# Kernel optimization log

Hardware: AMD Instinct MI355X
Metric: run time of the kernel (lower is better)

Reference implementation:

```python
import jax, jax.numpy as jnp
import numpy as np

N_NODES = 50000
N_EDGES = 800000  # undirected edge count E0
D_FEAT = 64
K_STEPS = 10
LAMBDA = 3.0


def setup_inputs() -> dict:
    key = jax.random.key(0)
    k1, k2, k3 = jax.random.split(key, 3)
    x = jax.random.normal(k1, (N_NODES, D_FEAT), dtype=jnp.float32)
    edge_src = jax.random.randint(k2, (N_EDGES,), 0, N_NODES)
    edge_dst = jax.random.randint(k3, (N_EDGES,), 0, N_NODES)
    return {"x": x, "edge_src": edge_src, "edge_dst": edge_dst}


def _forward(x, edge_src, edge_dst):
    N, D = x.shape
    # --- symmetric adjacency (directed edge list, both orientations) ---
    row = jnp.concatenate([edge_src, edge_dst])
    col = jnp.concatenate([edge_dst, edge_src])
    # degree with self loops (fill_diag/add_self_loops weight 1), shared by
    # gcn_norm and inc_norm in the original code
    deg = jax.ops.segment_sum(jnp.ones(row.shape[0], x.dtype), row, num_segments=N) + 1.0
    dis = deg ** -0.5  # deg_inv_sqrt, [N]
    # gcn-normalized adjacency weights D^-1/2 (A+I) D^-1/2
    w = dis[row] * dis[col]          # off-diagonal edge weights [2*E0]
    w_self = dis * dis               # self-loop weights [N]

    def adj_mv(v):  # edge_index @ v
        return jax.ops.segment_sum(w[:, None] * v[col], row, num_segments=N) + w_self[:, None] * v

    # --- normalized incidence matrix (one row per undirected edge) ---
    r = jnp.maximum(edge_src, edge_dst)  # row_index after row>=col mask
    c = jnp.minimum(edge_src, edge_dst)
    a = dis[r]  # +1 entry scaled by deg_inv_sqrt of column r
    b = dis[c]  # -1 entry scaled by deg_inv_sqrt of column c

    def inc_mv(v):  # inc_mat @ v -> [E0, D]
        return a[:, None] * v[r] - b[:, None] * v[c]

    def incT_mv(z):  # inc_mat.t() @ z -> [N, D]
        return (jax.ops.segment_sum(a[:, None] * z, r, num_segments=N)
                - jax.ops.segment_sum(b[:, None] * z, c, num_segments=N))

    def l21_projection(z):
        rn = jnp.linalg.norm(z, axis=1)                 # row L2 norms [E0]
        s = jnp.minimum(rn, LAMBDA)
        s = jnp.where(rn > 0, s / jnp.where(rn > 0, rn, 1.0), s)
        return s[:, None] * z

    hh = x
    z0 = jnp.zeros((edge_src.shape[0], D), x.dtype)

    def step(carry, _):
        xk, zk = carry
        y = 0.25 * hh + 0.75 * adj_mv(xk)
        x_bar = y - 0.25 * incT_mv(zk)
        z_bar = zk + 2.0 * inc_mv(x_bar)
        zk = l21_projection(z_bar)
        xk = y - 0.25 * incT_mv(zk)
        return (xk, zk), None

    (xK, _), _ = jax.lax.scan(step, (x, z0), None, length=K_STEPS)
    return xK


def reference(x, edge_src, edge_dst):
    return _forward(x, edge_src, edge_dst)
```

## Files before the change

kernel.cpp:

```cpp
#include <hip/hip_runtime.h>
#include <hip/hip_fp16.h>
#include <math.h>

constexpr int NN = 50000;
constexpr int NE = 800000;
constexpr int KS = 10;
constexpr float LAM = 3.0f;

constexpr int SCAN_NB = (NN + 255) / 256;
constexpr int NODE_NB = NN * 64 / 256;


__global__ __launch_bounds__(256) void countRC_kernel(
    const int* __restrict__ src, const int* __restrict__ dst,
    int* __restrict__ cR, int* __restrict__ cC) {
  int e = blockIdx.x * 256 + threadIdx.x;
  if (e >= NE) return;
  int s = src[e], d = dst[e];
  int r = s > d ? s : d;
  int c = s > d ? d : s;
  atomicAdd(&cR[r], 1);
  atomicAdd(&cC[c], 1);
}

__global__ __launch_bounds__(256) void dis_kernel(
    const int* __restrict__ cR, const int* __restrict__ cC,
    float* __restrict__ dis) {
  int i = blockIdx.x * 256 + threadIdx.x;
  if (i < NN) dis[i] = 1.0f / sqrtf((float)(cR[i] + cC[i] + 1));
}

__global__ __launch_bounds__(256) void half_copy_kernel(
    const float* __restrict__ X, __half* __restrict__ XH) {
  int i = blockIdx.x * 256 + threadIdx.x;
  if (i >= NN * 16) return;
  float4 v = ((const float4*)X)[i];
  __half2 h0 = __floats2half2_rn(v.x, v.y);
  __half2 h1 = __floats2half2_rn(v.z, v.w);
  uint2 o;
  o.x = *(const unsigned*)&h0;
  o.y = *(const unsigned*)&h1;
  ((uint2*)XH)[i] = o;
}


__global__ __launch_bounds__(256) void scanA_kernel(
    const int* __restrict__ cnt, int* __restrict__ bsum) {
  __shared__ int sm[256];
  int t = threadIdx.x;
  int i = blockIdx.x * 256 + t;
  int v = (i < NN) ? cnt[i] : 0;
  sm[t] = v;
  __syncthreads();
  for (int off = 128; off > 0; off >>= 1) {
    if (t < off) sm[t] += sm[t + off];
    __syncthreads();
  }
  if (t == 0) bsum[blockIdx.x] = sm[0];
}

__global__ __launch_bounds__(256) void scanB_kernel(
    int* __restrict__ bsum, int* __restrict__ boff) {
  __shared__ int sm[256];
  int t = threadIdx.x;
  int v = (t < SCAN_NB) ? bsum[t] : 0;
  sm[t] = v;
  __syncthreads();
  for (int off = 1; off < 256; off <<= 1) {
    int a = (t >= off) ? sm[t - off] : 0;
    __syncthreads();
    sm[t] += a;
    __syncthreads();
  }
  if (t < SCAN_NB) boff[t] = sm[t] - v;
}

__global__ __launch_bounds__(256) void scanC_kernel(
    const int* __restrict__ cnt, const int* __restrict__ boff,
    int* __restrict__ ptr, int* __restrict__ cur) {
  __shared__ int sm[256];
  int t = threadIdx.x;
  int i = blockIdx.x * 256 + t;
  int v = (i < NN) ? cnt[i] : 0;
  sm[t] = v;
  __syncthreads();
  for (int off = 1; off < 256; off <<= 1) {
    int a = (t >= off) ? sm[t - off] : 0;
    __syncthreads();
    sm[t] += a;
    __syncthreads();
  }
  if (i < NN) {
    int ex = boff[blockIdx.x] + sm[t] - v;
    ptr[i] = ex;
    cur[i] = ex;
    if (i == NN - 1) ptr[NN] = ex + v;
  }
}

__global__ __launch_bounds__(256) void sortscatter_kernel(
    const int* __restrict__ src, const int* __restrict__ dst,
    const float* __restrict__ dis,
    int* __restrict__ urR, int* __restrict__ uC,
    int2* __restrict__ cb8, int2* __restrict__ cEnt) {
  int e = blockIdx.x * 256 + threadIdx.x;
  if (e >= NE) return;
  int s = src[e], d = dst[e];
  int r = s > d ? s : d;
  int c = s > d ? d : s;
  int p = atomicAdd(&urR[r], 1);
  cb8[p] = make_int2(c, __float_as_int(dis[c]));
  int q = atomicAdd(&uC[c], 1);
  cEnt[q] = make_int2(r, p);
}


template <int FIRST>
__global__ __launch_bounds__(256) void adj_kernel(
    const __half* __restrict__ XH, const float* __restrict__ H,
    const float* __restrict__ U, const float* __restrict__ dis,
    const int* __restrict__ rPtr, const int* __restrict__ cPtr,
    const int2* __restrict__ cEnt, const int2* __restrict__ cb8,
    float* __restrict__ XB, __half* __restrict__ XBh) {
  int w = (int)((blockIdx.x * 256u + threadIdx.x) >> 6);
  if (w >= NN) return;
  int lane = threadIdx.x & 63;
  int g = lane >> 4, l = lane & 15;
  const uint2* XH2 = (const uint2*)XH;
  int rb = rPtr[w], lenR = rPtr[w + 1] - rb;
  int cb = cPtr[w], lenC = cPtr[w + 1] - cb;
  int total = lenR + lenC;
  int lr1 = lenR > 0 ? lenR - 1 : 0;
  int lc1 = lenC > 0 ? lenC - 1 : 0;
  float ax = 0.f, ay = 0.f, az = 0.f, aw = 0.f;

#define ADJ_FETCH(T, NB, WT)                                         \
  {                                                                  \
    int tr = (T) < lr1 ? (T) : lr1;                                  \
    int tc = (T) - lenR; tc = tc > 0 ? tc : 0; tc = tc < lc1 ? tc : lc1; \
    int2 rcv = cb8[rb + tr];                                         \
    int2 ce = cEnt[cb + tc];                                         \
    bool isR = (T) < lenR;                                           \
    NB = isR ? rcv.x : ce.x;                                         \
    WT = isR ? __int_as_float(rcv.y) : dis[ce.x];                    \
  }
#define ADJ_ACC(XV, W)                                               \
  {                                                                  \
    float2 p = __half22float2(*(const __half2*)&XV.x);               \
    float2 q = __half22float2(*(const __half2*)&XV.y);               \
    ax = fmaf(W, p.x, ax); ay = fmaf(W, p.y, ay);                    \
    az = fmaf(W, q.x, az); aw = fmaf(W, q.y, aw);                    \
  }

  int t = g;
  for (; t + 12 < total; t += 16) {
    int n0, n1, n2, n3; float w0, w1, w2, w3;
    ADJ_FETCH(t, n0, w0);
    ADJ_FETCH(t + 4, n1, w1);
    ADJ_FETCH(t + 8, n2, w2);
    ADJ_FETCH(t + 12, n3, w3);
    uint2 x0 = XH2[n0 * 16 + l];
    uint2 x1 = XH2[n1 * 16 + l];
    uint2 x2 = XH2[n2 * 16 + l];
    uint2 x3 = XH2[n3 * 16 + l];
    ADJ_ACC(x0, w0);
    ADJ_ACC(x1, w1);
    ADJ_ACC(x2, w2);
    ADJ_ACC(x3, w3);
  }
  for (; t < total; t += 4) {
    int n0; float w0;
    ADJ_FETCH(t, n0, w0);
    uint2 x0 = XH2[n0 * 16 + l];
    ADJ_ACC(x0, w0);
  }
#undef ADJ_FETCH
#undef ADJ_ACC

  ax += __shfl_xor(ax, 16, 64); ay += __shfl_xor(ay, 16, 64);
  az += __shfl_xor(az, 16, 64); aw += __shfl_xor(aw, 16, 64);
  ax += __shfl_xor(ax, 32, 64); ay += __shfl_xor(ay, 32, 64);
  az += __shfl_xor(az, 32, 64); aw += __shfl_xor(aw, 32, 64);
  if (g == 0) {
    float di = dis[w];
    int idx = w * 16 + l;
    uint2 xsu = XH2[idx];
    float2 xsa = __half22float2(*(const __half2*)&xsu.x);
    float2 xsb = __half22float2(*(const __half2*)&xsu.y);
    float4 h4 = ((const float4*)H)[idx];
    float4 y4;
    y4.x = 0.25f * h4.x + 0.75f * di * fmaf(di, xsa.x, ax);
    y4.y = 0.25f * h4.y + 0.75f * di * fmaf(di, xsa.y, ay);
    y4.z = 0.25f * h4.z + 0.75f * di * fmaf(di, xsb.x, az);
    y4.w = 0.25f * h4.w + 0.75f * di * fmaf(di, xsb.y, aw);
    float4 xb;
    if (FIRST) {
      xb = y4;
    } else {
      float4 u4 = ((const float4*)U)[idx];
      xb.x = y4.x - 0.25f * u4.x;
      xb.y = y4.y - 0.25f * u4.y;
      xb.z = y4.z - 0.25f * u4.z;
      xb.w = y4.w - 0.25f * u4.w;
    }
    ((float4*)XB)[idx] = xb;
    __half2 hb0 = __floats2half2_rn(xb.x, xb.y);
    __half2 hb1 = __floats2half2_rn(xb.z, xb.w);
    uint2 ob;
    ob.x = *(const unsigned*)&hb0;
    ob.y = *(const unsigned*)&hb1;
    ((uint2*)XBh)[idx] = ob;
  }
}

template <int FIRST>
__global__ __launch_bounds__(256) void zupd_kernel(
    __half* __restrict__ Z, const __half* __restrict__ XBh,
    const float* __restrict__ dis,
    const int* __restrict__ rPtr, const int2* __restrict__ cb8,
    float* __restrict__ U1) {
  int i = (int)((blockIdx.x * 256u + threadIdx.x) >> 6);
  if (i >= NN) return;
  int w = (i & 1) ? (NN - 1 - (i >> 1)) : (i >> 1);
  int lane = threadIdx.x & 63;
  int g = lane >> 4, l = lane & 15;
  const uint2* X2 = (const uint2*)XBh;
  uint2* Z2 = (uint2*)Z;
  int rb = rPtr[w], re = rPtr[w + 1];
  float a2 = 2.0f * dis[w];
  uint2 xwu = X2[w * 16 + l];
  float2 xwa = __half22float2(*(const __half2*)&xwu.x);
  float2 xwb = __half22float2(*(const __half2*)&xwu.y);
  float tx = a2 * xwa.x, ty = a2 * xwa.y;
  float tz = a2 * xwb.x, tw = a2 * xwb.y;
  float sx = 0.f, sy = 0.f, sz = 0.f, sw = 0.f;

#define Z_PROC(E, CV, XCU, ZU)                                       \
  {                                                                  \
    float b2 = 2.0f * __int_as_float(CV.y);                          \
    float2 xca = __half22float2(*(const __half2*)&XCU.x);            \
    float2 xcb = __half22float2(*(const __half2*)&XCU.y);            \
    float zx, zy, zz, zw;                                            \
    if (FIRST) {                                                     \
      zx = zy = zz = zw = 0.f;                                       \
    } else {                                                         \
      float2 f0 = __half22float2(*(const __half2*)&ZU.x);            \
      float2 f1 = __half22float2(*(const __half2*)&ZU.y);            \
      zx = f0.x; zy = f0.y; zz = f1.x; zw = f1.y;                    \
    }                                                                \
    zx += tx - b2 * xca.x;                                           \
    zy += ty - b2 * xca.y;                                           \
    zz += tz - b2 * xcb.x;                                           \
    zw += tw - b2 * xcb.y;                                           \
    float ss = zx * zx + zy * zy + zz * zz + zw * zw;                \
    ss += __shfl_xor(ss, 1, 64);                                     \
    ss += __shfl_xor(ss, 2, 64);                                     \
    ss += __shfl_xor(ss, 4, 64);                                     \
    ss += __shfl_xor(ss, 8, 64);                                     \
    float rn = sqrtf(ss);                                            \
    float sc = (rn > LAM) ? (LAM / rn) : 1.0f;                       \
    zx *= sc; zy *= sc; zz *= sc; zw *= sc;                          \
    __half2 o0 = __floats2half2_rn(zx, zy);                          \
    __half2 o1 = __floats2half2_rn(zz, zw);                          \
    uint2 outu;                                                      \
    outu.x = *(const unsigned*)&o0;                                  \
    outu.y = *(const unsigned*)&o1;                                  \
    Z2[(E) * 16 + l] = outu;                                         \
    sx += zx; sy += zy; sz += zz; sw += zw;                          \
  }

  int e = rb + g;
  for (; e + 4 < re; e += 8) {
    int2 cv0 = cb8[e];
    int2 cv1 = cb8[e + 4];
    uint2 xc0 = X2[cv0.x * 16 + l];
    uint2 xc1 = X2[cv1.x * 16 + l];
    uint2 zu0, zu1;
    if (!FIRST) {
      zu0 = Z2[e * 16 + l];
      zu1 = Z2[(e + 4) * 16 + l];
    }
    Z_PROC(e, cv0, xc0, zu0);
    Z_PROC(e + 4, cv1, xc1, zu1);
  }
  if (e < re) {
    int2 cv0 = cb8[e];
    uint2 xc0 = X2[cv0.x * 16 + l];
    uint2 zu0;
    if (!FIRST) zu0 = Z2[e * 16 + l];
    Z_PROC(e, cv0, xc0, zu0);
  }
#undef Z_PROC

  sx += __shfl_xor(sx, 16, 64); sy += __shfl_xor(sy, 16, 64);
  sz += __shfl_xor(sz, 16, 64); sw += __shfl_xor(sw, 16, 64);
  sx += __shfl_xor(sx, 32, 64); sy += __shfl_xor(sy, 32, 64);
  sz += __shfl_xor(sz, 32, 64); sw += __shfl_xor(sw, 32, 64);
  if (g == 0) {
    ((float4*)U1)[w * 16 + l] = make_float4(sx, sy, sz, sw);
  }
}

template <int FIRST, int LAST>
__global__ __launch_bounds__(256) void cside_kernel(
    const __half* __restrict__ Z, const float* __restrict__ XB,
    const float* __restrict__ dis,
    const int* __restrict__ cPtr, const int2* __restrict__ cEnt,
    const float* __restrict__ U1, float* __restrict__ U,
    float* __restrict__ Xout, __half* __restrict__ XH) {
  int i = (int)((blockIdx.x * 256u + threadIdx.x) >> 6);
  if (i >= NN) return;
  int w = (i & 1) ? (NN - 1 - (i >> 1)) : (i >> 1);
  int lane = threadIdx.x & 63;
  int g = lane >> 4, l = lane & 15;
  const uint2* Z2 = (const uint2*)Z;
  int cb = cPtr[w], ce = cPtr[w + 1];
  float sx = 0.f, sy = 0.f, sz = 0.f, sw = 0.f;
  int j = cb + g;
  for (; j + 12 < ce; j += 16) {
    int e0 = cEnt[j].y;
    int e1 = cEnt[j + 4].y;
    int e2 = cEnt[j + 8].y;
    int e3 = cEnt[j + 12].y;
    uint2 zu0 = Z2[e0 * 16 + l];
    uint2 zu1 = Z2[e1 * 16 + l];
    uint2 zu2 = Z2[e2 * 16 + l];
    uint2 zu3 = Z2[e3 * 16 + l];
    float2 a0 = __half22float2(*(const __half2*)&zu0.x);
    float2 b0 = __half22float2(*(const __half2*)&zu0.y);
    float2 a1 = __half22float2(*(const __half2*)&zu1.x);
    float2 b1 = __half22float2(*(const __half2*)&zu1.y);
    float2 a2 = __half22float2(*(const __half2*)&zu2.x);
    float2 b2 = __half22float2(*(const __half2*)&zu2.y);
    float2 a3 = __half22float2(*(const __half2*)&zu3.x);
    float2 b3 = __half22float2(*(const __half2*)&zu3.y);
    sx += a0.x + a1.x + a2.x + a3.x;
    sy += a0.y + a1.y + a2.y + a3.y;
    sz += b0.x + b1.x + b2.x + b3.x;
    sw += b0.y + b1.y + b2.y + b3.y;
  }
  for (; j < ce; j += 4) {
    int e0 = cEnt[j].y;
    uint2 zu0 = Z2[e0 * 16 + l];
    float2 a0 = __half22float2(*(const __half2*)&zu0.x);
    float2 b0 = __half22float2(*(const __half2*)&zu0.y);
    sx += a0.x; sy += a0.y; sz += b0.x; sw += b0.y;
  }
  sx += __shfl_xor(sx, 16, 64); sy += __shfl_xor(sy, 16, 64);
  sz += __shfl_xor(sz, 16, 64); sw += __shfl_xor(sw, 16, 64);
  sx += __shfl_xor(sx, 32, 64); sy += __shfl_xor(sy, 32, 64);
  sz += __shfl_xor(sz, 32, 64); sw += __shfl_xor(sw, 32, 64);
  if (g == 0) {
    float di = dis[w];
    int idx = w * 16 + l;
    float4 u1 = ((const float4*)U1)[idx];
    float4 u;
    u.x = di * (u1.x - sx);
    u.y = di * (u1.y - sy);
    u.z = di * (u1.z - sz);
    u.w = di * (u1.w - sw);
    float4 xb = ((const float4*)XB)[idx];
    float4 y4;
    if (FIRST) {
      y4 = xb;
    } else {
      float4 uo = ((const float4*)U)[idx];
      y4.x = xb.x + 0.25f * uo.x;
      y4.y = xb.y + 0.25f * uo.y;
      y4.z = xb.z + 0.25f * uo.z;
      y4.w = xb.w + 0.25f * uo.w;
    }
    float4 o;
    o.x = y4.x - 0.25f * u.x;
    o.y = y4.y - 0.25f * u.y;
    o.z = y4.z - 0.25f * u.z;
    o.w = y4.w - 0.25f * u.w;
    if (LAST) {
      ((float4*)Xout)[idx] = o;
    } else {
      ((float4*)U)[idx] = u;
      __half2 h0 = __floats2half2_rn(o.x, o.y);
      __half2 h1 = __floats2half2_rn(o.z, o.w);
      uint2 oh;
      oh.x = *(const unsigned*)&h0;
      oh.y = *(const unsigned*)&h1;
      ((uint2*)XH)[idx] = oh;
    }
  }
}


extern "C" void kernel_launch(void* const* d_in, const int* in_sizes, int n_in,
                              void* d_out, int out_size, void* d_ws, size_t ws_size,
                              hipStream_t stream) {
  const float* x  = (const float*)d_in[0];
  const int* esrc = (const int*)d_in[1];
  const int* edst = (const int*)d_in[2];
  float* out = (float*)d_out;

  char* base = (char*)d_ws;
  size_t off = 0;
  auto carve = [&](size_t bytes) -> void* {
    void* p = base + off;
    off += (bytes + 255) & ~(size_t)255;
    return p;
  };
  __half* Z   = (__half*)carve((size_t)NE * 64 * 2);
  float* XB   = (float*)carve((size_t)NN * 64 * 4);
  float* U    = (float*)carve((size_t)NN * 64 * 4);
  float* U1   = (float*)carve((size_t)NN * 64 * 4);
  __half* XH  = (__half*)carve((size_t)NN * 64 * 2);
  __half* XBh = (__half*)carve((size_t)NN * 64 * 2);
  float* dis = (float*)carve((size_t)NN * 4);
  int* cR  = (int*)carve((size_t)NN * 4);
  int* cC  = (int*)carve((size_t)NN * 4);
  int* rPtr = (int*)carve((size_t)(NN + 1) * 4);
  int* cPtr = (int*)carve((size_t)(NN + 1) * 4);
  int* urR = (int*)carve((size_t)NN * 4);
  int* uC  = (int*)carve((size_t)NN * 4);
  int* bsum = (int*)carve((size_t)SCAN_NB * 4);
  int* boff = (int*)carve((size_t)SCAN_NB * 4);
  int2* cb8  = (int2*)carve((size_t)(NE + 4) * 8);
  int2* cEnt = (int2*)carve((size_t)(NE + 4) * 8);
  (void)ws_size; (void)in_sizes; (void)n_in; (void)out_size;

  hipMemsetAsync(cR, 0, NN * 4, stream);
  hipMemsetAsync(cC, 0, NN * 4, stream);

  const int edgeGrid = (NE + 255) / 256;
  countRC_kernel<<<edgeGrid, 256, 0, stream>>>(esrc, edst, cR, cC);
  dis_kernel<<<(NN + 255) / 256, 256, 0, stream>>>(cR, cC, dis);
  half_copy_kernel<<<(NN * 16 + 255) / 256, 256, 0, stream>>>(x, XH);
  scanA_kernel<<<SCAN_NB, 256, 0, stream>>>(cR, bsum);
  scanB_kernel<<<1, 256, 0, stream>>>(bsum, boff);
  scanC_kernel<<<SCAN_NB, 256, 0, stream>>>(cR, boff, rPtr, urR);
  scanA_kernel<<<SCAN_NB, 256, 0, stream>>>(cC, bsum);
  scanB_kernel<<<1, 256, 0, stream>>>(bsum, boff);
  scanC_kernel<<<SCAN_NB, 256, 0, stream>>>(cC, boff, cPtr, uC);
  sortscatter_kernel<<<edgeGrid, 256, 0, stream>>>(esrc, edst, dis, urR, uC,
                                                   cb8, cEnt);

  for (int k = 0; k < KS; ++k) {
    if (k == 0)
      adj_kernel<1><<<NODE_NB, 256, 0, stream>>>(XH, x, U, dis, rPtr, cPtr,
                                                 cEnt, cb8, XB, XBh);
    else
      adj_kernel<0><<<NODE_NB, 256, 0, stream>>>(XH, x, U, dis, rPtr, cPtr,
                                                 cEnt, cb8, XB, XBh);

    if (k == 0)
      zupd_kernel<1><<<NODE_NB, 256, 0, stream>>>(Z, XBh, dis, rPtr, cb8, U1);
    else
      zupd_kernel<0><<<NODE_NB, 256, 0, stream>>>(Z, XBh, dis, rPtr, cb8, U1);

    if (k == 0)
      cside_kernel<1, 0><<<NODE_NB, 256, 0, stream>>>(Z, XB, dis, cPtr, cEnt,
                                                      U1, U, out, XH);
    else if (k == KS - 1)
      cside_kernel<0, 1><<<NODE_NB, 256, 0, stream>>>(Z, XB, dis, cPtr, cEnt,
                                                      U1, U, out, XH);
    else
      cside_kernel<0, 0><<<NODE_NB, 256, 0, stream>>>(Z, XB, dis, cPtr, cEnt,
                                                      U1, U, out, XH);
  }
}
```

Before: 1.360 ms.

## Precompute merged adjacency list with weights and deepen zupd unroll

Result: no change. 1.377 ms (+1.3%).

```diff
diff --git a/kernel.cpp b/kernel.cpp
--- a/kernel.cpp
+++ b/kernel.cpp
@@ -114,36 +114,47 @@
   cEnt[q] = make_int2(r, p);
 }
 
+__global__ __launch_bounds__(256) void adjm_kernel(
+    const int* __restrict__ rPtr, const int* __restrict__ cPtr,
+    const int2* __restrict__ cb8, const int2* __restrict__ cEnt,
+    const float* __restrict__ dis, int2* __restrict__ adjM) {
+  int w = (int)((blockIdx.x * 256u + threadIdx.x) >> 6);
+  if (w >= NN) return;
+  int lane = threadIdx.x & 63;
+  int rb = rPtr[w], lenR = rPtr[w + 1] - rb;
+  int cb = cPtr[w], lenC = cPtr[w + 1] - cb;
+  int total = lenR + lenC;
+  int ab = rb + cb;
+  for (int t = lane; t < total; t += 64) {
+    int2 m;
+    if (t < lenR) {
+      m = cb8[rb + t];
+    } else {
+      int rr = cEnt[cb + t - lenR].x;
+      m = make_int2(rr, __float_as_int(dis[rr]));
+    }
+    adjM[ab + t] = m;
+  }
+}
+
 
 template <int FIRST>
 __global__ __launch_bounds__(256) void adj_kernel(
     const __half* __restrict__ XH, const float* __restrict__ H,
     const float* __restrict__ U, const float* __restrict__ dis,
     const int* __restrict__ rPtr, const int* __restrict__ cPtr,
-    const int2* __restrict__ cEnt, const int2* __restrict__ cb8,
+    const int2* __restrict__ adjM,
     float* __restrict__ XB, __half* __restrict__ XBh) {
   int w = (int)((blockIdx.x * 256u + threadIdx.x) >> 6);
   if (w >= NN) return;
   int lane = threadIdx.x & 63;
   int g = lane >> 4, l = lane & 15;
   const uint2* XH2 = (const uint2*)XH;
-  int rb = rPtr[w], lenR = rPtr[w + 1] - rb;
-  int cb = cPtr[w], lenC = cPtr[w + 1] - cb;
-  int total = lenR + lenC;
-  int lr1 = lenR > 0 ? lenR - 1 : 0;
-  int lc1 = lenC > 0 ? lenC - 1 : 0;
+  int rb = rPtr[w], cb = cPtr[w];
+  int ab = rb + cb;
+  int total = rPtr[w + 1] + cPtr[w + 1] - ab;
   float ax = 0.f, ay = 0.f, az = 0.f, aw = 0.f;
 
-#define ADJ_FETCH(T, NB, WT)                                         \
-  {                                                                  \
-    int tr = (T) < lr1 ? (T) : lr1;                                  \
-    int tc = (T) - lenR; tc = tc > 0 ? tc : 0; tc = tc < lc1 ? tc : lc1; \
-    int2 rcv = cb8[rb + tr];                                         \
-    int2 ce = cEnt[cb + tc];                                         \
-    bool isR = (T) < lenR;                                           \
-    NB = isR ? rcv.x : ce.x;                                         \
-    WT = isR ? __int_as_float(rcv.y) : dis[ce.x];                    \
-  }
 #define ADJ_ACC(XV, W)                                               \
   {                                                                  \
     float2 p = __half22float2(*(const __half2*)&XV.x);               \
@@ -154,27 +165,27 @@
 
   int t = g;
   for (; t + 12 < total; t += 16) {
-    int n0, n1, n2, n3; float w0, w1, w2, w3;
-    ADJ_FETCH(t, n0, w0);
-    ADJ_FETCH(t + 4, n1, w1);
-    ADJ_FETCH(t + 8, n2, w2);
-    ADJ_FETCH(t + 12, n3, w3);
-    uint2 x0 = XH2[n0 * 16 + l];
-    uint2 x1 = XH2[n1 * 16 + l];
-    uint2 x2 = XH2[n2 * 16 + l];
-    uint2 x3 = XH2[n3 * 16 + l];
+    int2 m0 = adjM[ab + t];
+    int2 m1 = adjM[ab + t + 4];
+    int2 m2 = adjM[ab + t + 8];
+    int2 m3 = adjM[ab + t + 12];
+    uint2 x0 = XH2[m0.x * 16 + l];
+    uint2 x1 = XH2[m1.x * 16 + l];
+    uint2 x2 = XH2[m2.x * 16 + l];
+    uint2 x3 = XH2[m3.x * 16 + l];
+    float w0 = __int_as_float(m0.y), w1 = __int_as_float(m1.y);
+    float w2 = __int_as_float(m2.y), w3 = __int_as_float(m3.y);
     ADJ_ACC(x0, w0);
     ADJ_ACC(x1, w1);
     ADJ_ACC(x2, w2);
     ADJ_ACC(x3, w3);
   }
   for (; t < total; t += 4) {
-    int n0; float w0;
-    ADJ_FETCH(t, n0, w0);
-    uint2 x0 = XH2[n0 * 16 + l];
+    int2 m0 = adjM[ab + t];
+    uint2 x0 = XH2[m0.x * 16 + l];
+    float w0 = __int_as_float(m0.y);
     ADJ_ACC(x0, w0);
   }
-#undef ADJ_FETCH
 #undef ADJ_ACC
 
   ax += __shfl_xor(ax, 16, 64); ay += __shfl_xor(ay, 16, 64);
@@ -270,20 +281,28 @@
   }
 
   int e = rb + g;
-  for (; e + 4 < re; e += 8) {
+  for (; e + 12 < re; e += 16) {
     int2 cv0 = cb8[e];
     int2 cv1 = cb8[e + 4];
+    int2 cv2 = cb8[e + 8];
+    int2 cv3 = cb8[e + 12];
     uint2 xc0 = X2[cv0.x * 16 + l];
     uint2 xc1 = X2[cv1.x * 16 + l];
-    uint2 zu0, zu1;
+    uint2 xc2 = X2[cv2.x * 16 + l];
+    uint2 xc3 = X2[cv3.x * 16 + l];
+    uint2 zu0, zu1, zu2, zu3;
     if (!FIRST) {
       zu0 = Z2[e * 16 + l];
       zu1 = Z2[(e + 4) * 16 + l];
+      zu2 = Z2[(e + 8) * 16 + l];
+      zu3 = Z2[(e + 12) * 16 + l];
     }
     Z_PROC(e, cv0, xc0, zu0);
     Z_PROC(e + 4, cv1, xc1, zu1);
-  }
-  if (e < re) {
+    Z_PROC(e + 8, cv2, xc2, zu2);
+    Z_PROC(e + 12, cv3, xc3, zu3);
+  }
+  for (; e < re; e += 4) {
     int2 cv0 = cb8[e];
     uint2 xc0 = X2[cv0.x * 16 + l];
     uint2 zu0;
@@ -422,6 +441,7 @@
   int* boff = (int*)carve((size_t)SCAN_NB * 4);
   int2* cb8  = (int2*)carve((size_t)(NE + 4) * 8);
   int2* cEnt = (int2*)carve((size_t)(NE + 4) * 8);
+  int2* adjM = (int2*)carve((size_t)(2 * NE + 4) * 8);
   (void)ws_size; (void)in_sizes; (void)n_in; (void)out_size;
 
   hipMemsetAsync(cR, 0, NN * 4, stream);
@@ -439,14 +459,15 @@
   scanC_kernel<<<SCAN_NB, 256, 0, stream>>>(cC, boff, cPtr, uC);
   sortscatter_kernel<<<edgeGrid, 256, 0, stream>>>(esrc, edst, dis, urR, uC,
                                                    cb8, cEnt);
+  adjm_kernel<<<NODE_NB, 256, 0, stream>>>(rPtr, cPtr, cb8, cEnt, dis, adjM);
 
   for (int k = 0; k < KS; ++k) {
     if (k == 0)
       adj_kernel<1><<<NODE_NB, 256, 0, stream>>>(XH, x, U, dis, rPtr, cPtr,
-                                                 cEnt, cb8, XB, XBh);
+                                                 adjM, XB, XBh);
     else
       adj_kernel<0><<<NODE_NB, 256, 0, stream>>>(XH, x, U, dis, rPtr, cPtr,
-                                                 cEnt, cb8, XB, XBh);
+                                                 adjM, XB, XBh);
 
     if (k == 0)
       zupd_kernel<1><<<NODE_NB, 256, 0, stream>>>(Z, XBh, dis, rPtr, cb8, U1);
```
